# Kernel tuning notes

Measured on AMD Instinct MI355X. Metric: run time of the kernel, lower is better.

Reference implementation:

```python
import jax, jax.numpy as jnp
import numpy as np

HEADS = 4
HEAD_DIM = 32  # hidden_dim // num_heads = 128 // 4
HIDDEN = 128
NEG_SLOPE = 0.2  # GATConv default


def gat_conv(x, src, dst, W, att_src, att_dst, bias):
    """PyG GATConv (concat=True, default negative_slope=0.2), eval mode.
    x: [N, F_in], src/dst: [E] (self-loops already included)."""
    N = x.shape[0]
    h = (x @ W).reshape(N, HEADS, HEAD_DIM)               # [N, H, D]
    a_src = jnp.einsum('nhd,hd->nh', h, att_src)          # [N, H]
    a_dst = jnp.einsum('nhd,hd->nh', h, att_dst)
    e = jax.nn.leaky_relu(a_src[src] + a_dst[dst], NEG_SLOPE)  # [E, H]
    # numerically stable softmax over incoming edges of each dst node
    m = jax.ops.segment_max(e, dst, num_segments=N)
    m = jnp.where(jnp.isfinite(m), m, 0.0)
    p = jnp.exp(e - m[dst])
    denom = jax.ops.segment_sum(p, dst, num_segments=N)
    alpha = p / (denom[dst] + 1e-16)                      # [E, H]
    out = jax.ops.segment_sum(h[src] * alpha[..., None], dst, num_segments=N)
    return out.reshape(N, HEADS * HEAD_DIM) + bias


def setup_inputs() -> dict:
    key = jax.random.key(0)
    ks = jax.random.split(key, 20)
    n_news, n_tweets, E = 20000, 80000, 1600000
    N = n_news + n_tweets
    s = 0.05
    inp = {
        'x_news': jax.random.normal(ks[0], (n_news, 768), jnp.float32),
        'x_tweets': jax.random.normal(ks[1], (n_tweets, 512), jnp.float32),
        'edge_index': jax.random.randint(ks[2], (2, E), 0, N, jnp.int32),
        'W_news': jax.random.normal(ks[3], (768, HIDDEN), jnp.float32) * s,
        'b_news': jnp.zeros((HIDDEN,), jnp.float32),
        'W_tw': jax.random.normal(ks[4], (512, HIDDEN), jnp.float32) * s,
        'b_tw': jnp.zeros((HIDDEN,), jnp.float32),
        'gat1_W': jax.random.normal(ks[5], (HIDDEN, HIDDEN), jnp.float32) * s,
        'gat1_as': jax.random.normal(ks[6], (HEADS, HEAD_DIM), jnp.float32) * s,
        'gat1_ad': jax.random.normal(ks[7], (HEADS, HEAD_DIM), jnp.float32) * s,
        'gat1_b': jnp.zeros((HIDDEN,), jnp.float32),
        'gat2_W': jax.random.normal(ks[8], (HIDDEN, HIDDEN), jnp.float32) * s,
        'gat2_as': jax.random.normal(ks[9], (HEADS, HEAD_DIM), jnp.float32) * s,
        'gat2_ad': jax.random.normal(ks[10], (HEADS, HEAD_DIM), jnp.float32) * s,
        'gat2_b': jnp.zeros((HIDDEN,), jnp.float32),
        'Wc1': jax.random.normal(ks[11], (HIDDEN, HIDDEN // 2), jnp.float32) * s,
        'bc1': jnp.zeros((HIDDEN // 2,), jnp.float32),
        'Wc2': jax.random.normal(ks[12], (HIDDEN // 2, 2), jnp.float32) * s,
        'bc2': jnp.zeros((2,), jnp.float32),
    }
    return inp


def reference(x_news, x_tweets, edge_index, W_news, b_news, W_tw, b_tw,
              gat1_W, gat1_as, gat1_ad, gat1_b,
              gat2_W, gat2_as, gat2_ad, gat2_b,
              Wc1, bc1, Wc2, bc2):
    n_news = x_news.shape[0]
    # encoders (dropout is identity in eval)
    h_news = jax.nn.relu(x_news @ W_news + b_news)
    h_tw = jax.nn.relu(x_tweets @ W_tw + b_tw)
    x = jnp.concatenate([h_news, h_tw], axis=0)           # [N, 128]
    N = x.shape[0]
    # GATConv default: add self-loops
    loops = jnp.arange(N, dtype=edge_index.dtype)
    src = jnp.concatenate([edge_index[0], loops])
    dst = jnp.concatenate([edge_index[1], loops])
    x = jax.nn.elu(gat_conv(x, src, dst, gat1_W, gat1_as, gat1_ad, gat1_b))
    x = jax.nn.elu(gat_conv(x, src, dst, gat2_W, gat2_as, gat2_ad, gat2_b))
    news_emb = x[:n_news]
    out = jax.nn.relu(news_emb @ Wc1 + bc1) @ Wc2 + bc2   # [n_news, 2]
    return out
```

## Files before the change

### kernel.cpp

```cpp
#include <hip/hip_runtime.h>
#include <hip/hip_bf16.h>
#include <type_traits>

typedef __attribute__((ext_vector_type(8))) short bf16x8;
typedef __attribute__((ext_vector_type(8))) unsigned short u16x8;
typedef __attribute__((ext_vector_type(4))) float f32x4;

__device__ __forceinline__ unsigned short f2b(float f) {
  union { float f; unsigned u; } c; c.f = f;
  return (unsigned short)((c.u + 0x7fffu + ((c.u >> 16) & 1u)) >> 16);
}
__device__ __forceinline__ float b2f(unsigned short v) {
  return __uint_as_float((unsigned)v << 16);
}

constexpr int BK = 64;
constexpr int LS = BK + 8;

template<int BM, int K, int ACT, int LOGITS, typename AT>
__device__ __forceinline__ void gemm_body(
    int bid, unsigned short* As, unsigned short* Bs,
    const AT* __restrict__ A, int M,
    const unsigned short* __restrict__ WT, const float* __restrict__ bias,
    unsigned short* __restrict__ C,
    const float* __restrict__ att_src, const float* __restrict__ att_dst,
    float* __restrict__ a_src, float* __restrict__ a_dst)
{
  constexpr int WTN = 32;
  constexpr int MF = BM / 16;
  constexpr int NF = 2;
  const int t = threadIdx.x;
  const int lane = t & 63;
  const int wc = t >> 6;
  const long row0 = (long)bid * BM;

  f32x4 acc[MF][NF] = {};

  for (int k0 = 0; k0 < K; k0 += BK) {
    if constexpr (std::is_same<AT, float>::value) {
#pragma unroll
      for (int i = 0; i < BM / 16; ++i) {
        int idx = t + i * 256;
        int r = idx >> 4;
        int kq = idx & 15;
        long gr = row0 + r; if (gr >= M) gr = M - 1;
        const float4 v = *(const float4*)(A + gr * K + k0 + kq * 4);
        ushort4 b;
        b.x = f2b(v.x); b.y = f2b(v.y); b.z = f2b(v.z); b.w = f2b(v.w);
        *(ushort4*)(&As[r * LS + kq * 4]) = b;
      }
    } else {
#pragma unroll
      for (int i = 0; i < BM / 32; ++i) {
        int idx = t + i * 256;
        int r = idx >> 3;
        int k8 = idx & 7;
        long gr = row0 + r; if (gr >= M) gr = M - 1;
        u16x8 v = *(const u16x8*)(A + gr * K + k0 + k8 * 8);
        *(u16x8*)(&As[r * LS + k8 * 8]) = v;
      }
    }
#pragma unroll
    for (int i = 0; i < 4; ++i) {
      int idx = t + i * 256;
      int col = idx >> 3;
      int k8 = idx & 7;
      u16x8 v = *(const u16x8*)(WT + (long)col * K + k0 + k8 * 8);
      *(u16x8*)(&Bs[col * LS + k8 * 8]) = v;
    }
    __syncthreads();
#pragma unroll
    for (int kk = 0; kk < BK; kk += 32) {
      const int koff = kk + (lane >> 4) * 8;
      bf16x8 af[MF], bfr[NF];
#pragma unroll
      for (int n = 0; n < NF; ++n)
        bfr[n] = *(const bf16x8*)(&Bs[(wc * WTN + n * 16 + (lane & 15)) * LS + koff]);
#pragma unroll
      for (int m = 0; m < MF; ++m)
        af[m] = *(const bf16x8*)(&As[(m * 16 + (lane & 15)) * LS + koff]);
#pragma unroll
      for (int m = 0; m < MF; ++m)
#pragma unroll
        for (int n = 0; n < NF; ++n)
          acc[m][n] = __builtin_amdgcn_mfma_f32_16x16x32_bf16(af[m], bfr[n], acc[m][n], 0, 0, 0);
    }
    __syncthreads();
  }

  float asv[NF], adv[NF];
  if (LOGITS) {
#pragma unroll
    for (int n = 0; n < NF; ++n) {
      int dim = n * 16 + (lane & 15);
      asv[n] = att_src[wc * 32 + dim];
      adv[n] = att_dst[wc * 32 + dim];
    }
  }

#pragma unroll
  for (int m = 0; m < MF; ++m) {
#pragma unroll
    for (int j = 0; j < 4; ++j) {
      long gr = row0 + m * 16 + (lane >> 4) * 4 + j;
      if (gr < M) {
#pragma unroll
        for (int n = 0; n < NF; ++n) {
          int c = wc * WTN + n * 16 + (lane & 15);
          float v = acc[m][n][j];
          if (bias) v += bias[c];
          if (ACT == 1) v = fmaxf(v, 0.f);
          C[gr * 128 + c] = f2b(v);
        }
      }
      if (LOGITS) {
        float sa = fmaf(acc[m][0][j], asv[0], acc[m][1][j] * asv[1]);
        float da = fmaf(acc[m][0][j], adv[0], acc[m][1][j] * adv[1]);
#pragma unroll
        for (int off = 1; off < 16; off <<= 1) {
          sa += __shfl_xor(sa, off);
          da += __shfl_xor(da, off);
        }
        if ((lane & 15) == 0 && gr < M) {
          a_src[gr * 4 + wc] = sa;
          a_dst[gr * 4 + wc] = da;
        }
      }
    }
  }
}

__device__ __forceinline__ void hist_body(int bid, int* cnt, const int* __restrict__ dst,
                                          int E, int* __restrict__ bcount, int nb)
{
  int t = threadIdx.x;
  for (int b = t; b < 512; b += 256) cnt[b] = 0;
  __syncthreads();
  int e0 = bid * 8192;
  for (int i = 0; i < 32; ++i) {
    int e = e0 + i * 256 + t;
    if (e < E) atomicAdd(&cnt[dst[e] >> 8], 1);
  }
  __syncthreads();
  for (int b = t; b < nb; b += 256) {
    int c = cnt[b];
    if (c > 0) atomicAdd(&bcount[b], c);
  }
}

__device__ __forceinline__ void scatter_body(int bid, int* s, const int* __restrict__ src,
                                             const int* __restrict__ dst, int E,
                                             int* __restrict__ bcur, int2* __restrict__ pairs)
{
  int* cnt = s;
  int* base = s + 512;
  int* rcur = s + 1024;
  int t = threadIdx.x;
  for (int b = t; b < 512; b += 256) { cnt[b] = 0; rcur[b] = 0; }
  __syncthreads();
  int e0 = bid * 8192;
  for (int i = 0; i < 32; ++i) {
    int e = e0 + i * 256 + t;
    if (e < E) atomicAdd(&cnt[dst[e] >> 8], 1);
  }
  __syncthreads();
  for (int b = t; b < 512; b += 256) {
    int c = cnt[b];
    if (c > 0) base[b] = atomicAdd(&bcur[b], c);
  }
  __syncthreads();
  for (int i = 0; i < 32; ++i) {
    int e = e0 + i * 256 + t;
    if (e < E) {
      int d = dst[e];
      int b = d >> 8;
      int off = atomicAdd(&rcur[b], 1);
      int2 p; p.x = src[e]; p.y = d;
      pairs[base[b] + off] = p;
    }
  }
}

__global__ __launch_bounds__(256) void mega1_kernel(
    int nb_tw, int nb_news,
    const float* __restrict__ x_tw, int n_tw, const unsigned short* __restrict__ WT_tw,
    const float* __restrict__ b_tw, unsigned short* __restrict__ out_tw,
    const float* __restrict__ x_news, int n_news, const unsigned short* __restrict__ WT_news,
    const float* __restrict__ b_news, unsigned short* __restrict__ out_news,
    const int* __restrict__ dst, int E, int* __restrict__ bcount, int nb)
{
  __shared__ unsigned short sh[(64 + 128) * LS];
  int bid = blockIdx.x;
  if (bid < nb_tw) {
    gemm_body<64, 512, 1, 0, float>(bid, sh, sh + 64 * LS, x_tw, n_tw, WT_tw, b_tw, out_tw,
                                    nullptr, nullptr, nullptr, nullptr);
  } else if (bid < nb_tw + nb_news) {
    gemm_body<32, 768, 1, 0, float>(bid - nb_tw, sh, sh + 32 * LS, x_news, n_news, WT_news,
                                    b_news, out_news, nullptr, nullptr, nullptr, nullptr);
  } else {
    hist_body(bid - nb_tw - nb_news, (int*)sh, dst, E, bcount, nb);
  }
}

__global__ __launch_bounds__(256) void mega3_kernel(
    int nb_gemm,
    const unsigned short* __restrict__ x_feat, int N, const unsigned short* __restrict__ WT_g1,
    unsigned short* __restrict__ h_feat,
    const float* __restrict__ g1as, const float* __restrict__ g1ad,
    float* __restrict__ a_src, float* __restrict__ a_dst,
    const int* __restrict__ src, const int* __restrict__ dst, int E,
    int* __restrict__ bcur, int2* __restrict__ pairs)
{
  __shared__ unsigned short sh[(64 + 128) * LS];
  int bid = blockIdx.x;
  if (bid < nb_gemm) {
    gemm_body<64, 128, 0, 1, unsigned short>(bid, sh, sh + 64 * LS, x_feat, N, WT_g1, nullptr,
                                             h_feat, g1as, g1ad, a_src, a_dst);
  } else {
    scatter_body(bid - nb_gemm, (int*)sh, src, dst, E, bcur, pairs);
  }
}

template<int BM, int K, int ACT, int LOGITS, typename AT>
__global__ __launch_bounds__(256) void gemm_kernel(
    const AT* __restrict__ A, int M,
    const unsigned short* __restrict__ WT, const float* __restrict__ bias,
    unsigned short* __restrict__ C,
    const float* __restrict__ att_src, const float* __restrict__ att_dst,
    float* __restrict__ a_src, float* __restrict__ a_dst)
{
  __shared__ unsigned short sh[(BM + 128) * LS];
  gemm_body<BM, K, ACT, LOGITS, AT>(blockIdx.x, sh, sh + BM * LS, A, M, WT, bias, C,
                                    att_src, att_dst, a_src, a_dst);
}

__global__ void transpose_all_kernel(const float* __restrict__ W0, unsigned short* __restrict__ T0,
                                     const float* __restrict__ W1, unsigned short* __restrict__ T1,
                                     const float* __restrict__ W2, unsigned short* __restrict__ T2,
                                     const float* __restrict__ W3, unsigned short* __restrict__ T3)
{
  int r = blockIdx.x * 256 + threadIdx.x;
  if (r < 128 * 768) { int c = r / 768, k = r - c * 768; T0[r] = f2b(W0[(size_t)k * 128 + c]); return; }
  r -= 128 * 768;
  if (r < 128 * 512) { int c = r / 512, k = r - c * 512; T1[r] = f2b(W1[(size_t)k * 128 + c]); return; }
  r -= 128 * 512;
  if (r < 128 * 128) { T2[r] = f2b(W2[(size_t)(r & 127) * 128 + (r >> 7)]); return; }
  r -= 128 * 128;
  if (r < 128 * 128) { T3[r] = f2b(W3[(size_t)(r & 127) * 128 + (r >> 7)]); return; }
}

__global__ __launch_bounds__(512) void bucket_scan_kernel(const int* __restrict__ bcount, int nb, int E,
                                                          int* __restrict__ bstart, int* __restrict__ bcur,
                                                          int* __restrict__ row_ptr, int N)
{
  __shared__ int s[512];
  int t = threadIdx.x;
  int my = (t < nb) ? bcount[t] : 0;
  s[t] = my;
  __syncthreads();
  for (int off = 1; off < 512; off <<= 1) {
    int v = (t >= off) ? s[t - off] : 0;
    __syncthreads();
    s[t] += v;
    __syncthreads();
  }
  int excl = s[t] - my;
  if (t < nb) { bstart[t] = excl; bcur[t] = excl; }
  if (t == 0) { bstart[nb] = E; row_ptr[N] = E; }
}

__global__ __launch_bounds__(256) void bucket_csr_kernel(const int2* __restrict__ pairs,
                                                         const int* __restrict__ bstart, int N,
                                                         int* __restrict__ row_ptr, int* __restrict__ col_idx)
{
  __shared__ int cnt[256];
  __shared__ int excl[256];
  __shared__ int cur[256];
  int t = threadIdx.x;
  int nodebase = blockIdx.x << 8;
  int start = bstart[blockIdx.x];
  int size = bstart[blockIdx.x + 1] - start;
  cnt[t] = 0;
  __syncthreads();
  for (int i = t; i < size; i += 256)
    atomicAdd(&cnt[pairs[start + i].y & 255], 1);
  __syncthreads();
  int my = cnt[t];
  excl[t] = my;
  __syncthreads();
  for (int off = 1; off < 256; off <<= 1) {
    int v = (t >= off) ? excl[t - off] : 0;
    __syncthreads();
    excl[t] += v;
    __syncthreads();
  }
  int ex = excl[t] - my;
  if (nodebase + t < N) row_ptr[nodebase + t] = start + ex;
  excl[t] = ex;
  cur[t] = 0;
  __syncthreads();
  for (int i = t; i < size; i += 256) {
    int2 p = pairs[start + i];
    int local = p.y & 255;
    int pos = start + excl[local] + atomicAdd(&cur[local], 1);
    col_idx[pos] = p.x;
  }
}

__global__ void gat_aggregate_kernel(const unsigned short* __restrict__ h, const float* __restrict__ a_src,
                                     const float* __restrict__ a_dst, const int* __restrict__ row_ptr,
                                     const int* __restrict__ col_idx, const float* __restrict__ bias,
                                     int Nproc, unsigned short* __restrict__ out)
{
  int n = (blockIdx.x * blockDim.x + threadIdx.x) >> 6;
  int lane = threadIdx.x & 63;
  if (n >= Nproc) return;
  const int sub = lane >> 4;
  const int sl = lane & 15;
  const int head = sl >> 2;
  const int beg = row_ptr[n], end = row_ptr[n + 1];
  const float adst = a_dst[(size_t)n * 4 + head];

  float slf = a_src[(size_t)n * 4 + head] + adst;
  slf = fmaxf(slf, 0.2f * slf);
  float ps = (sub == 0) ? __expf(slf) : 0.f;
  float denom = ps;
  float acc[8];
  {
    const u16x8 hs = *(const u16x8*)(h + (size_t)n * 128 + 8 * sl);
#pragma unroll
    for (int j = 0; j < 8; ++j) acc[j] = ps * b2f(hs[j]);
  }

  int e = beg + sub;
  for (; e + 4 < end; e += 8) {
    const int s0 = col_idx[e];
    const int s1 = col_idx[e + 4];
    const u16x8 h0 = *(const u16x8*)(h + (size_t)s0 * 128 + 8 * sl);
    const u16x8 h1 = *(const u16x8*)(h + (size_t)s1 * 128 + 8 * sl);
    float l0 = a_src[(size_t)s0 * 4 + head] + adst;
    float l1 = a_src[(size_t)s1 * 4 + head] + adst;
    l0 = fmaxf(l0, 0.2f * l0);
    l1 = fmaxf(l1, 0.2f * l1);
    const float p0 = __expf(l0);
    const float p1 = __expf(l1);
    denom += p0 + p1;
#pragma unroll
    for (int j = 0; j < 8; ++j) {
      acc[j] = fmaf(p0, b2f(h0[j]), acc[j]);
      acc[j] = fmaf(p1, b2f(h1[j]), acc[j]);
    }
  }
  if (e < end) {
    const int s = col_idx[e];
    const u16x8 hv = *(const u16x8*)(h + (size_t)s * 128 + 8 * sl);
    float lg = a_src[(size_t)s * 4 + head] + adst;
    lg = fmaxf(lg, 0.2f * lg);
    const float p = __expf(lg);
    denom += p;
#pragma unroll
    for (int j = 0; j < 8; ++j) acc[j] = fmaf(p, b2f(hv[j]), acc[j]);
  }

#pragma unroll
  for (int j = 0; j < 8; ++j) {
    acc[j] += __shfl_xor(acc[j], 16);
    acc[j] += __shfl_xor(acc[j], 32);
  }
  denom += __shfl_xor(denom, 16);
  denom += __shfl_xor(denom, 32);

  if (sub == 0) {
    const float inv = 1.0f / (denom + 1e-16f);
    const float4 b0 = *(const float4*)(bias + 8 * sl);
    const float4 b1 = *(const float4*)(bias + 8 * sl + 4);
    float o[8];
    o[0] = acc[0] * inv + b0.x; o[1] = acc[1] * inv + b0.y;
    o[2] = acc[2] * inv + b0.z; o[3] = acc[3] * inv + b0.w;
    o[4] = acc[4] * inv + b1.x; o[5] = acc[5] * inv + b1.y;
    o[6] = acc[6] * inv + b1.z; o[7] = acc[7] * inv + b1.w;
    u16x8 r;
#pragma unroll
    for (int j = 0; j < 8; ++j) {
      float v = (o[j] > 0.f) ? o[j] : expm1f(o[j]);
      r[j] = f2b(v);
    }
    *(u16x8*)(out + (size_t)n * 128 + 8 * sl) = r;
  }
}

__global__ void classifier_kernel(const unsigned short* __restrict__ x, const float* __restrict__ Wc1,
                                  const float* __restrict__ bc1, const float* __restrict__ Wc2,
                                  const float* __restrict__ bc2, float* __restrict__ out, int M)
{
  int row = (blockIdx.x * blockDim.x + threadIdx.x) >> 6;
  int lane = threadIdx.x & 63;
  if (row >= M) return;
  const unsigned short* xr = x + (size_t)row * 128;
  float c = 0.f;
#pragma unroll 8
  for (int k = 0; k < 128; k += 2) {
    unsigned v = *(const unsigned*)(xr + k);
    c = fmaf(__uint_as_float(v << 16), Wc1[k * 64 + lane], c);
    c = fmaf(__uint_as_float(v & 0xffff0000u), Wc1[(k + 1) * 64 + lane], c);
  }
  c += bc1[lane];
  c = fmaxf(c, 0.f);
  float o0 = c * Wc2[lane * 2 + 0];
  float o1 = c * Wc2[lane * 2 + 1];
#pragma unroll
  for (int off = 1; off < 64; off <<= 1) {
    o0 += __shfl_xor(o0, off);
    o1 += __shfl_xor(o1, off);
  }
  if (lane == 0) {
    out[(size_t)row * 2 + 0] = o0 + bc2[0];
    out[(size_t)row * 2 + 1] = o1 + bc2[1];
  }
}

extern "C" void kernel_launch(void* const* d_in, const int* in_sizes, int n_in,
                              void* d_out, int out_size, void* d_ws, size_t ws_size,
                              hipStream_t stream)
{
  const float* x_news = (const float*)d_in[0];
  const float* x_tw   = (const float*)d_in[1];
  const int*   ei     = (const int*)d_in[2];
  const float* W_news = (const float*)d_in[3];
  const float* b_news = (const float*)d_in[4];
  const float* W_tw   = (const float*)d_in[5];
  const float* b_tw   = (const float*)d_in[6];
  const float* g1W  = (const float*)d_in[7];
  const float* g1as = (const float*)d_in[8];
  const float* g1ad = (const float*)d_in[9];
  const float* g1b  = (const float*)d_in[10];
  const float* g2W  = (const float*)d_in[11];
  const float* g2as = (const float*)d_in[12];
  const float* g2ad = (const float*)d_in[13];
  const float* g2b  = (const float*)d_in[14];
  const float* Wc1  = (const float*)d_in[15];
  const float* bc1  = (const float*)d_in[16];
  const float* Wc2  = (const float*)d_in[17];
  const float* bc2  = (const float*)d_in[18];

  const int n_news = in_sizes[0] / 768;
  const int n_tw   = in_sizes[1] / 512;
  const int N = n_news + n_tw;
  const int E = in_sizes[2] / 2;
  const int* src = ei;
  const int* dst = ei + E;
  const int nb = (N + 255) >> 8;

  char* ws = (char*)d_ws;
  size_t off = 0;
  auto alloc = [&](size_t bytes) -> void* {
    void* p = ws + off;
    off += (bytes + 255) & ~(size_t)255;
    return p;
  };
  unsigned short* x_feat = (unsigned short*)alloc((size_t)N * 128 * 2);
  unsigned short* h_feat = (unsigned short*)alloc((size_t)N * 128 * 2);
  float* a_src   = (float*)alloc((size_t)N * 4 * 4);
  float* a_dst   = (float*)alloc((size_t)N * 4 * 4);
  int*   row_ptr = (int*)alloc((size_t)(N + 1) * 4);
  int*   col_idx = (int*)alloc((size_t)E * 4);
  int2*  pairs   = (int2*)alloc((size_t)E * 8);
  int*   bcount  = (int*)alloc(2048);
  int*   bstart  = (int*)alloc(2052);
  int*   bcur    = (int*)alloc(2048);
  unsigned short* WT_news = (unsigned short*)alloc((size_t)128 * 768 * 2);
  unsigned short* WT_tw   = (unsigned short*)alloc((size_t)128 * 512 * 2);
  unsigned short* WT_g1   = (unsigned short*)alloc((size_t)128 * 128 * 2);
  unsigned short* WT_g2   = (unsigned short*)alloc((size_t)128 * 128 * 2);

  hipMemsetAsync(bcount, 0, 2048, stream);

  transpose_all_kernel<<<768, 256, 0, stream>>>(W_news, WT_news, W_tw, WT_tw, g1W, WT_g1, g2W, WT_g2);

  const int nb_tw = (n_tw + 63) / 64;
  const int nb_news = (n_news + 31) / 32;
  const int nb_hist = (E + 8191) / 8192;
  mega1_kernel<<<nb_tw + nb_news + nb_hist, 256, 0, stream>>>(
      nb_tw, nb_news,
      x_tw, n_tw, WT_tw, b_tw, x_feat + (size_t)n_news * 128,
      x_news, n_news, WT_news, b_news, x_feat,
      dst, E, bcount, nb);

  bucket_scan_kernel<<<1, 512, 0, stream>>>(bcount, nb, E, bstart, bcur, row_ptr, N);

  const int nb_g = (N + 63) / 64;
  const int nb_hist2 = (E + 8191) / 8192;
  mega3_kernel<<<nb_g + nb_hist2, 256, 0, stream>>>(
      nb_g, x_feat, N, WT_g1, h_feat, g1as, g1ad, a_src, a_dst,
      src, dst, E, bcur, pairs);

  bucket_csr_kernel<<<nb, 256, 0, stream>>>(pairs, bstart, N, row_ptr, col_idx);

  gat_aggregate_kernel<<<(N + 3) / 4, 256, 0, stream>>>(h_feat, a_src, a_dst, row_ptr, col_idx, g1b, N, x_feat);

  gemm_kernel<64, 128, 0, 1, unsigned short><<<nb_g, 256, 0, stream>>>(
      x_feat, N, WT_g2, nullptr, h_feat, g2as, g2ad, a_src, a_dst);
  gat_aggregate_kernel<<<(n_news + 3) / 4, 256, 0, stream>>>(h_feat, a_src, a_dst, row_ptr, col_idx, g2b, n_news, x_feat);

  classifier_kernel<<<(n_news + 3) / 4, 256, 0, stream>>>(x_feat, Wc1, bc1, Wc2, bc2, (float*)d_out, n_news);
}
```

Measured before the change: 309.4 us.

## Read GEMM weights directly from global, enlarge K-tile, fuse final aggregation with classifier

The GEMM body no longer stages the weight matrix in shared memory. Each wave loads its B fragments straight from global/L2, and the K tile grows to 256 (encoders) or 128 (GAT layers). This cuts the number of __syncthreads rounds and the LDS traffic, and the A loads are split into a load phase and a store phase so more loads are in flight. The second GAT aggregation is fused with the classifier MLP, which removes one kernel launch and the write and re-read of the news embeddings. The cost is more scattered global reads of the weights per wave, and larger LDS tiles that may lower occupancy.

```diff
diff --git a/kernel.cpp b/kernel.cpp
--- a/kernel.cpp
+++ b/kernel.cpp
@@ -14,85 +14,92 @@
   return __uint_as_float((unsigned)v << 16);
 }
 
-constexpr int BK = 64;
-constexpr int LS = BK + 8;
-
-template<int BM, int K, int ACT, int LOGITS, typename AT>
+template<int BM, int K, int BKT, int ACT, int LOGITS, typename AT>
 __device__ __forceinline__ void gemm_body(
-    int bid, unsigned short* As, unsigned short* Bs,
+    int bid, unsigned short* As,
     const AT* __restrict__ A, int M,
     const unsigned short* __restrict__ WT, const float* __restrict__ bias,
     unsigned short* __restrict__ C,
     const float* __restrict__ att_src, const float* __restrict__ att_dst,
     float* __restrict__ a_src, float* __restrict__ a_dst)
 {
-  constexpr int WTN = 32;
+  constexpr int LSW = BKT + 8;
   constexpr int MF = BM / 16;
   constexpr int NF = 2;
   const int t = threadIdx.x;
   const int lane = t & 63;
   const int wc = t >> 6;
+  const int fr = lane & 15;
+  const int kb = lane >> 4;
   const long row0 = (long)bid * BM;
 
   f32x4 acc[MF][NF] = {};
 
-  for (int k0 = 0; k0 < K; k0 += BK) {
+  for (int k0 = 0; k0 < K; k0 += BKT) {
     if constexpr (std::is_same<AT, float>::value) {
-#pragma unroll
-      for (int i = 0; i < BM / 16; ++i) {
+      constexpr int NU = BM * (BKT / 4) / 256;
+      float4 rv[NU];
+#pragma unroll
+      for (int i = 0; i < NU; ++i) {
         int idx = t + i * 256;
-        int r = idx >> 4;
-        int kq = idx & 15;
+        int r = idx / (BKT / 4);
+        int kq = idx % (BKT / 4);
         long gr = row0 + r; if (gr >= M) gr = M - 1;
-        const float4 v = *(const float4*)(A + gr * K + k0 + kq * 4);
+        rv[i] = *(const float4*)(A + gr * K + k0 + kq * 4);
+      }
+#pragma unroll
+      for (int i = 0; i < NU; ++i) {
+        int idx = t + i * 256;
+        int r = idx / (BKT / 4);
+        int kq = idx % (BKT / 4);
         ushort4 b;
-        b.x = f2b(v.x); b.y = f2b(v.y); b.z = f2b(v.z); b.w = f2b(v.w);
-        *(ushort4*)(&As[r * LS + kq * 4]) = b;
+        b.x = f2b(rv[i].x); b.y = f2b(rv[i].y); b.z = f2b(rv[i].z); b.w = f2b(rv[i].w);
+        *(ushort4*)(&As[r * LSW + kq * 4]) = b;
       }
     } else {
-#pragma unroll
-      for (int i = 0; i < BM / 32; ++i) {
+      constexpr int NU = BM * (BKT / 8) / 256;
+      u16x8 rv[NU];
+#pragma unroll
+      for (int i = 0; i < NU; ++i) {
         int idx = t + i * 256;
-        int r = idx >> 3;
-        int k8 = idx & 7;
+        int r = idx / (BKT / 8);
+        int k8 = idx % (BKT / 8);
         long gr = row0 + r; if (gr >= M) gr = M - 1;
-        u16x8 v = *(const u16x8*)(A + gr * K + k0 + k8 * 8);
-        *(u16x8*)(&As[r * LS + k8 * 8]) = v;
+        rv[i] = *(const u16x8*)(A + gr * K + k0 + k8 * 8);
       }
-    }
-#pragma unroll
-    for (int i = 0; i < 4; ++i) {
-      int idx = t + i * 256;
-      int col = idx >> 3;
-      int k8 = idx & 7;
-      u16x8 v = *(const u16x8*)(WT + (long)col * K + k0 + k8 * 8);
-      *(u16x8*)(&Bs[col * LS + k8 * 8]) = v;
+#pragma unroll
+      for (int i = 0; i < NU; ++i) {
+        int idx = t + i * 256;
+        int r = idx / (BKT / 8);
+        int k8 = idx % (BKT / 8);
+        *(u16x8*)(&As[r * LSW + k8 * 8]) = rv[i];
+      }
     }
     __syncthreads();
 #pragma unroll
-    for (int kk = 0; kk < BK; kk += 32) {
-      const int koff = kk + (lane >> 4) * 8;
+    for (int kk = 0; kk < BKT; kk += 32) {
+      const int koff = kk + kb * 8;
       bf16x8 af[MF], bfr[NF];
 #pragma unroll
       for (int n = 0; n < NF; ++n)
-        bfr[n] = *(const bf16x8*)(&Bs[(wc * WTN + n * 16 + (lane & 15)) * LS + koff]);
+        bfr[n] = *(const bf16x8*)(WT + (long)(wc * 32 + n * 16 + fr) * K + k0 + koff);
 #pragma unroll
       for (int m = 0; m < MF; ++m)
-        af[m] = *(const bf16x8*)(&As[(m * 16 + (lane & 15)) * LS + koff]);
+        af[m] = *(const bf16x8*)(&As[(m * 16 + fr) * LSW + koff]);
 #pragma unroll
       for (int m = 0; m < MF; ++m)
 #pragma unroll
         for (int n = 0; n < NF; ++n)
           acc[m][n] = __builtin_amdgcn_mfma_f32_16x16x32_bf16(af[m], bfr[n], acc[m][n], 0, 0, 0);
     }
-    __syncthreads();
+    if (k0 + BKT < K) __syncthreads();
   }
 
   float asv[NF], adv[NF];
   if (LOGITS) {
 #pragma unroll
     for (int n = 0; n < NF; ++n) {
-      int dim = n * 16 + (lane & 15);
+      int dim = n * 16 + fr;
       asv[n] = att_src[wc * 32 + dim];
       adv[n] = att_dst[wc * 32 + dim];
     }
@@ -102,11 +109,11 @@
   for (int m = 0; m < MF; ++m) {
 #pragma unroll
     for (int j = 0; j < 4; ++j) {
-      long gr = row0 + m * 16 + (lane >> 4) * 4 + j;
+      long gr = row0 + m * 16 + kb * 4 + j;
       if (gr < M) {
 #pragma unroll
         for (int n = 0; n < NF; ++n) {
-          int c = wc * WTN + n * 16 + (lane & 15);
+          int c = wc * 32 + n * 16 + fr;
           float v = acc[m][n][j];
           if (bias) v += bias[c];
           if (ACT == 1) v = fmaxf(v, 0.f);
@@ -121,7 +128,7 @@
           sa += __shfl_xor(sa, off);
           da += __shfl_xor(da, off);
         }
-        if ((lane & 15) == 0 && gr < M) {
+        if (fr == 0 && gr < M) {
           a_src[gr * 4 + wc] = sa;
           a_dst[gr * 4 + wc] = da;
         }
@@ -189,14 +196,14 @@
     const float* __restrict__ b_news, unsigned short* __restrict__ out_news,
     const int* __restrict__ dst, int E, int* __restrict__ bcount, int nb)
 {
-  __shared__ unsigned short sh[(64 + 128) * LS];
+  __shared__ unsigned short sh[64 * (256 + 8)];
   int bid = blockIdx.x;
   if (bid < nb_tw) {
-    gemm_body<64, 512, 1, 0, float>(bid, sh, sh + 64 * LS, x_tw, n_tw, WT_tw, b_tw, out_tw,
-                                    nullptr, nullptr, nullptr, nullptr);
+    gemm_body<64, 512, 256, 1, 0, float>(bid, sh, x_tw, n_tw, WT_tw, b_tw, out_tw,
+                                         nullptr, nullptr, nullptr, nullptr);
   } else if (bid < nb_tw + nb_news) {
-    gemm_body<32, 768, 1, 0, float>(bid - nb_tw, sh, sh + 32 * LS, x_news, n_news, WT_news,
-                                    b_news, out_news, nullptr, nullptr, nullptr, nullptr);
+    gemm_body<32, 768, 256, 1, 0, float>(bid - nb_tw, sh, x_news, n_news, WT_news,
+                                         b_news, out_news, nullptr, nullptr, nullptr, nullptr);
   } else {
     hist_body(bid - nb_tw - nb_news, (int*)sh, dst, E, bcount, nb);
   }
@@ -211,17 +218,17 @@
     const int* __restrict__ src, const int* __restrict__ dst, int E,
     int* __restrict__ bcur, int2* __restrict__ pairs)
 {
-  __shared__ unsigned short sh[(64 + 128) * LS];
+  __shared__ unsigned short sh[64 * (128 + 8)];
   int bid = blockIdx.x;
   if (bid < nb_gemm) {
-    gemm_body<64, 128, 0, 1, unsigned short>(bid, sh, sh + 64 * LS, x_feat, N, WT_g1, nullptr,
-                                             h_feat, g1as, g1ad, a_src, a_dst);
+    gemm_body<64, 128, 128, 0, 1, unsigned short>(bid, sh, x_feat, N, WT_g1, nullptr,
+                                                  h_feat, g1as, g1ad, a_src, a_dst);
   } else {
     scatter_body(bid - nb_gemm, (int*)sh, src, dst, E, bcur, pairs);
   }
 }
 
-template<int BM, int K, int ACT, int LOGITS, typename AT>
+template<int BM, int K, int BKT, int ACT, int LOGITS, typename AT>
 __global__ __launch_bounds__(256) void gemm_kernel(
     const AT* __restrict__ A, int M,
     const unsigned short* __restrict__ WT, const float* __restrict__ bias,
@@ -229,9 +236,9 @@
     const float* __restrict__ att_src, const float* __restrict__ att_dst,
     float* __restrict__ a_src, float* __restrict__ a_dst)
 {
-  __shared__ unsigned short sh[(BM + 128) * LS];
-  gemm_body<BM, K, ACT, LOGITS, AT>(blockIdx.x, sh, sh + BM * LS, A, M, WT, bias, C,
-                                    att_src, att_dst, a_src, a_dst);
+  __shared__ unsigned short sh[BM * (BKT + 8)];
+  gemm_body<BM, K, BKT, ACT, LOGITS, AT>(blockIdx.x, sh, A, M, WT, bias, C,
+                                         att_src, att_dst, a_src, a_dst);
 }
 
 __global__ void transpose_all_kernel(const float* __restrict__ W0, unsigned short* __restrict__ T0,
@@ -389,20 +396,92 @@
   }
 }
 
-__global__ void classifier_kernel(const unsigned short* __restrict__ x, const float* __restrict__ Wc1,
-                                  const float* __restrict__ bc1, const float* __restrict__ Wc2,
-                                  const float* __restrict__ bc2, float* __restrict__ out, int M)
-{
-  int row = (blockIdx.x * blockDim.x + threadIdx.x) >> 6;
+__global__ void gat_agg_cls_kernel(const unsigned short* __restrict__ h, const float* __restrict__ a_src,
+                                   const float* __restrict__ a_dst, const int* __restrict__ row_ptr,
+                                   const int* __restrict__ col_idx, const float* __restrict__ bias,
+                                   int n_news,
+                                   const float* __restrict__ Wc1, const float* __restrict__ bc1,
+                                   const float* __restrict__ Wc2, const float* __restrict__ bc2,
+                                   float* __restrict__ out)
+{
+  int n = (blockIdx.x * blockDim.x + threadIdx.x) >> 6;
   int lane = threadIdx.x & 63;
-  if (row >= M) return;
-  const unsigned short* xr = x + (size_t)row * 128;
+  if (n >= n_news) return;
+  const int sub = lane >> 4;
+  const int sl = lane & 15;
+  const int head = sl >> 2;
+  const int beg = row_ptr[n], end = row_ptr[n + 1];
+  const float adst = a_dst[(size_t)n * 4 + head];
+
+  float slf = a_src[(size_t)n * 4 + head] + adst;
+  slf = fmaxf(slf, 0.2f * slf);
+  float ps = (sub == 0) ? __expf(slf) : 0.f;
+  float denom = ps;
+  float acc[8];
+  {
+    const u16x8 hs = *(const u16x8*)(h + (size_t)n * 128 + 8 * sl);
+#pragma unroll
+    for (int j = 0; j < 8; ++j) acc[j] = ps * b2f(hs[j]);
+  }
+
+  int e = beg + sub;
+  for (; e + 4 < end; e += 8) {
+    const int s0 = col_idx[e];
+    const int s1 = col_idx[e + 4];
+    const u16x8 h0 = *(const u16x8*)(h + (size_t)s0 * 128 + 8 * sl);
+    const u16x8 h1 = *(const u16x8*)(h + (size_t)s1 * 128 + 8 * sl);
+    float l0 = a_src[(size_t)s0 * 4 + head] + adst;
+    float l1 = a_src[(size_t)s1 * 4 + head] + adst;
+    l0 = fmaxf(l0, 0.2f * l0);
+    l1 = fmaxf(l1, 0.2f * l1);
+    const float p0 = __expf(l0);
+    const float p1 = __expf(l1);
+    denom += p0 + p1;
+#pragma unroll
+    for (int j = 0; j < 8; ++j) {
+      acc[j] = fmaf(p0, b2f(h0[j]), acc[j]);
+      acc[j] = fmaf(p1, b2f(h1[j]), acc[j]);
+    }
+  }
+  if (e < end) {
+    const int s = col_idx[e];
+    const u16x8 hv = *(const u16x8*)(h + (size_t)s * 128 + 8 * sl);
+    float lg = a_src[(size_t)s * 4 + head] + adst;
+    lg = fmaxf(lg, 0.2f * lg);
+    const float p = __expf(lg);
+    denom += p;
+#pragma unroll
+    for (int j = 0; j < 8; ++j) acc[j] = fmaf(p, b2f(hv[j]), acc[j]);
+  }
+
+#pragma unroll
+  for (int j = 0; j < 8; ++j) {
+    acc[j] += __shfl_xor(acc[j], 16);
+    acc[j] += __shfl_xor(acc[j], 32);
+  }
+  denom += __shfl_xor(denom, 16);
+  denom += __shfl_xor(denom, 32);
+
+  const float inv = 1.0f / (denom + 1e-16f);
+  const float4 b0 = *(const float4*)(bias + 8 * sl);
+  const float4 b1 = *(const float4*)(bias + 8 * sl + 4);
+  float o[8];
+  o[0] = acc[0] * inv + b0.x; o[1] = acc[1] * inv + b0.y;
+  o[2] = acc[2] * inv + b0.z; o[3] = acc[3] * inv + b0.w;
+  o[4] = acc[4] * inv + b1.x; o[5] = acc[5] * inv + b1.y;
+  o[6] = acc[6] * inv + b1.z; o[7] = acc[7] * inv + b1.w;
+#pragma unroll
+  for (int j = 0; j < 8; ++j)
+    o[j] = (o[j] > 0.f) ? o[j] : expm1f(o[j]);
+
   float c = 0.f;
-#pragma unroll 8
-  for (int k = 0; k < 128; k += 2) {
-    unsigned v = *(const unsigned*)(xr + k);
-    c = fmaf(__uint_as_float(v << 16), Wc1[k * 64 + lane], c);
-    c = fmaf(__uint_as_float(v & 0xffff0000u), Wc1[(k + 1) * 64 + lane], c);
+#pragma unroll
+  for (int j = 0; j < 8; ++j) {
+#pragma unroll
+    for (int kb = 0; kb < 16; ++kb) {
+      float x = __shfl(o[j], kb);
+      c = fmaf(x, Wc1[(kb * 8 + j) * 64 + lane], c);
+    }
   }
   c += bc1[lane];
   c = fmaxf(c, 0.f);
@@ -414,8 +493,8 @@
     o1 += __shfl_xor(o1, off);
   }
   if (lane == 0) {
-    out[(size_t)row * 2 + 0] = o0 + bc2[0];
-    out[(size_t)row * 2 + 1] = o1 + bc2[1];
+    out[(size_t)n * 2 + 0] = o0 + bc2[0];
+    out[(size_t)n * 2 + 1] = o1 + bc2[1];
   }
 }
 
@@ -489,8 +568,7 @@
   bucket_scan_kernel<<<1, 512, 0, stream>>>(bcount, nb, E, bstart, bcur, row_ptr, N);
 
   const int nb_g = (N + 63) / 64;
-  const int nb_hist2 = (E + 8191) / 8192;
-  mega3_kernel<<<nb_g + nb_hist2, 256, 0, stream>>>(
+  mega3_kernel<<<nb_g + nb_hist, 256, 0, stream>>>(
       nb_g, x_feat, N, WT_g1, h_feat, g1as, g1ad, a_src, a_dst,
       src, dst, E, bcur, pairs);
 
@@ -498,9 +576,9 @@
 
   gat_aggregate_kernel<<<(N + 3) / 4, 256, 0, stream>>>(h_feat, a_src, a_dst, row_ptr, col_idx, g1b, N, x_feat);
 
-  gemm_kernel<64, 128, 0, 1, unsigned short><<<nb_g, 256, 0, stream>>>(
+  gemm_kernel<64, 128, 128, 0, 1, unsigned short><<<nb_g, 256, 0, stream>>>(
       x_feat, N, WT_g2, nullptr, h_feat, g2as, g2ad, a_src, a_dst);
-  gat_aggregate_kernel<<<(n_news + 3) / 4, 256, 0, stream>>>(h_feat, a_src, a_dst, row_ptr, col_idx, g2b, n_news, x_feat);
-
-  classifier_kernel<<<(n_news + 3) / 4, 256, 0, stream>>>(x_feat, Wc1, bc1, Wc2, bc2, (float*)d_out, n_news);
-}
+  gat_agg_cls_kernel<<<(n_news + 3) / 4, 256, 0, stream>>>(
+      h_feat, a_src, a_dst, row_ptr, col_idx, g2b, n_news,
+      Wc1, bc1, Wc2, bc2, (float*)d_out);
+}
```

After: 341.2 us. 10.3% more time.
